# Optimization experiments

Measured on AMD Instinct MI355X. Metric: run time of the kernel, lower is better.

The kernel has to match this reference:

```python
import jax, jax.numpy as jnp
import numpy as np

N, H, C, E, R = 16384, 1024, 256, 16, 128
EPS = 1e-8


def setup_inputs() -> dict:
    key = jax.random.key(0)
    ks = jax.random.split(key, 8)
    s = 1.0 / np.sqrt(H)
    return {
        "x": jax.random.normal(ks[0], (N, H), jnp.float32),
        "Wd": jax.random.normal(ks[1], (H, C), jnp.float32) * s,
        "bd": jax.random.normal(ks[2], (C,), jnp.float32) * 0.01,
        "centroids": jax.random.uniform(ks[3], (E, C), jnp.float32),  # torch.rand
        "Wg": jax.random.normal(ks[4], (E, H, H), jnp.float32) * s,
        "bg": jax.random.normal(ks[5], (E, H), jnp.float32) * 0.01,
        "U": jax.random.normal(ks[6], (E, H, R), jnp.float32) * s,
        "V": jax.random.normal(ks[7], (E, R, H), jnp.float32) * (1.0 / np.sqrt(R)),
        "k": 2,
    }


def reference(x, Wd, bd, centroids, Wg, bg, U, V, k):
    # ---- Router ----
    distilled = jax.nn.gelu(x @ Wd + bd, approximate=False)          # [N, C]
    dn = distilled / jnp.maximum(
        jnp.linalg.norm(distilled, axis=-1, keepdims=True), EPS)
    cn = centroids / jnp.maximum(
        jnp.linalg.norm(centroids, axis=-1, keepdims=True), EPS)
    # cdist (euclidean) between dn [N,C] and cn [E,C]
    d2 = (jnp.sum(dn * dn, -1, keepdims=True)
          + jnp.sum(cn * cn, -1)[None, :]
          - 2.0 * (dn @ cn.T))                                        # [N, E]
    distances = jnp.sqrt(jnp.maximum(d2, 0.0))
    probabilities = jax.nn.softmax(-distances, axis=-1)               # [N, E]
    top_p, top_i = jax.lax.top_k(probabilities, k)                    # [N, k]
    # sparse combine weights: zero except at top-k experts
    combine = jnp.zeros((x.shape[0], E), x.dtype)
    combine = combine.at[jnp.arange(x.shape[0])[:, None], top_i].set(top_p)
    # ---- Expert dispatch: scan over experts (low-rank Highway blocks) ----
    def body(acc, params):
        Wg_e, bg_e, U_e, V_e, w_e = params
        gate = jax.nn.sigmoid(x @ Wg_e + bg_e)                        # [N, H]
        trans = (x @ U_e) @ V_e                                       # [N, H]
        y = gate * trans + (1.0 - gate) * x
        return acc + w_e[:, None] * y, None
    out, _ = jax.lax.scan(body, jnp.zeros_like(x),
                          (Wg, bg, U, V, combine.T))
    return out
```

## Files before the change

kernel.cpp:

```cpp
#include <hip/hip_runtime.h>
#include <hip/hip_bf16.h>
#include <hip/hip_fp16.h>
#include <cstdint>
#include <cstddef>

#define NTOK 16384
#define HD   1024
#define CD   256
#define NE   16
#define RD   128
#define MB2    272
#define LOGB   2176
#define EGRID  2304

typedef __attribute__((ext_vector_type(8))) short bf16x8;
typedef __attribute__((ext_vector_type(4))) float f32x4;
typedef unsigned short u16;
typedef unsigned int u32;

__device__ __forceinline__ u16 f2bf(float f) {
    u32 u = __float_as_uint(f);
    u32 r = (u + 0x7FFFu + ((u >> 16) & 1u)) >> 16;
    return (u16)r;
}

__device__ __forceinline__ void gload16(const void* g, void* lds) {
    __builtin_amdgcn_global_load_lds((const __attribute__((address_space(1))) void*)g,
                                     (__attribute__((address_space(3))) void*)lds,
                                     16, 0, 0);
}

__device__ __forceinline__ float wredsum(float v) {
#pragma unroll
    for (int m = 32; m >= 1; m >>= 1) v += __shfl_xor(v, m, 64);
    return v;
}

__global__ __launch_bounds__(64) void centroid_norm_kernel(
    const float* __restrict__ cen, float* __restrict__ cn, float* __restrict__ sncn)
{
    int e = blockIdx.x, l = threadIdx.x;
    float4 c = *(const float4*)&cen[e * CD + l * 4];
    float ss = wredsum(c.x * c.x + c.y * c.y + c.z * c.z + c.w * c.w);
    float den = fmaxf(sqrtf(ss), 1e-8f);
    float4 n;
    n.x = c.x / den; n.y = c.y / den; n.z = c.z / den; n.w = c.w / den;
    *(float4*)&cn[e * CD + l * 4] = n;
    float s2 = wredsum(n.x * n.x + n.y * n.y + n.z * n.z + n.w * n.w);
    if (l == 0) sncn[e] = s2;
}

__global__ __launch_bounds__(256, 4) void router_gemm_kernel(
    const float* __restrict__ x, const float* __restrict__ Wd,
    const float* __restrict__ bd, float* __restrict__ dT)
{
    __shared__ float lA[16][128];
    __shared__ float lB[16][64];
    int tid = threadIdx.x;
    int rb = (blockIdx.x >> 2) * 128;
    int cb = (blockIdx.x & 3) * 64;
    int tx = tid & 15, ty = tid >> 4;
    int arow = tid >> 1, akq = (tid & 1) * 8;
    int bk = tid >> 4, bc = (tid & 15) * 4;
    float acc[8][4];
#pragma unroll
    for (int i = 0; i < 8; ++i)
#pragma unroll
        for (int j = 0; j < 4; ++j) acc[i][j] = 0.f;

    for (int k0 = 0; k0 < HD; k0 += 16) {
        float4 a0 = *(const float4*)&x[(size_t)(rb + arow) * HD + k0 + akq];
        float4 a1 = *(const float4*)&x[(size_t)(rb + arow) * HD + k0 + akq + 4];
        float4 bv = *(const float4*)&Wd[(size_t)(k0 + bk) * CD + cb + bc];
        __syncthreads();
        lA[akq + 0][arow] = a0.x; lA[akq + 1][arow] = a0.y;
        lA[akq + 2][arow] = a0.z; lA[akq + 3][arow] = a0.w;
        lA[akq + 4][arow] = a1.x; lA[akq + 5][arow] = a1.y;
        lA[akq + 6][arow] = a1.z; lA[akq + 7][arow] = a1.w;
        *(float4*)&lB[bk][bc] = bv;
        __syncthreads();
#pragma unroll
        for (int kk = 0; kk < 16; ++kk) {
            float4 va0 = *(const float4*)&lA[kk][ty * 8];
            float4 va1 = *(const float4*)&lA[kk][ty * 8 + 4];
            float4 vb  = *(const float4*)&lB[kk][tx * 4];
            float ar[8] = {va0.x, va0.y, va0.z, va0.w, va1.x, va1.y, va1.z, va1.w};
            float br[4] = {vb.x, vb.y, vb.z, vb.w};
#pragma unroll
            for (int i = 0; i < 8; ++i)
#pragma unroll
                for (int j = 0; j < 4; ++j) acc[i][j] = fmaf(ar[i], br[j], acc[i][j]);
        }
    }
#pragma unroll
    for (int j = 0; j < 4; ++j) {
        int c = cb + tx * 4 + j;
        float b = bd[c];
        float g[8];
#pragma unroll
        for (int i = 0; i < 8; ++i) {
            float v = acc[i][j] + b;
            g[i] = 0.5f * v * (1.f + erff(v * 0.70710678118654752f));
        }
        float4 w0 = {g[0], g[1], g[2], g[3]};
        float4 w1 = {g[4], g[5], g[6], g[7]};
        *(float4*)&dT[(size_t)c * NTOK + rb + ty * 8] = w0;
        *(float4*)&dT[(size_t)c * NTOK + rb + ty * 8 + 4] = w1;
    }
}

__global__ __launch_bounds__(256) void router_score_kernel(
    const float* __restrict__ dT, const float* __restrict__ cn,
    const float* __restrict__ sncn, int* __restrict__ top_i,
    float* __restrict__ top_w, int* __restrict__ counts)
{
    __shared__ float lcn[NE][CD];
    __shared__ float sdot[NE][64];
    __shared__ float sss[64];
    __shared__ int hist[NE];
    int tid = threadIdx.x, lane = tid & 63, w = tid >> 6;
    for (int i = tid; i < NE * CD / 4; i += 256)
        ((float4*)&lcn[0][0])[i] = ((const float4*)cn)[i];
    if (tid < NE) hist[tid] = 0;
    __syncthreads();

    int tokbase = blockIdx.x * 64;
    const float* p = dT + tokbase + lane;
    int e0 = w * 4;
    float d0 = 0.f, d1 = 0.f, d2a = 0.f, d3 = 0.f, ss = 0.f;
#pragma unroll 4
    for (int k = 0; k < CD; ++k) {
        float v = p[(size_t)k * NTOK];
        ss = fmaf(v, v, ss);
        d0 = fmaf(v, lcn[e0 + 0][k], d0);
        d1 = fmaf(v, lcn[e0 + 1][k], d1);
        d2a = fmaf(v, lcn[e0 + 2][k], d2a);
        d3 = fmaf(v, lcn[e0 + 3][k], d3);
    }
    sdot[e0 + 0][lane] = d0;
    sdot[e0 + 1][lane] = d1;
    sdot[e0 + 2][lane] = d2a;
    sdot[e0 + 3][lane] = d3;
    if (w == 0) sss[lane] = ss;
    __syncthreads();

    if (tid < 64) {
        int tok = tokbase + tid;
        float ssv = sss[tid];
        float den = fmaxf(sqrtf(ssv), 1e-8f);
        float inv = 1.f / den;
        float sndn = (ssv * inv) * inv;
        float pr[NE];
#pragma unroll
        for (int e = 0; e < NE; ++e) {
            float dotn = sdot[e][tid] * inv;
            float dd2 = sndn + sncn[e] - 2.f * dotn;
            pr[e] = -sqrtf(fmaxf(dd2, 0.f));
        }
        float mx = pr[0];
#pragma unroll
        for (int e = 1; e < NE; ++e) mx = fmaxf(mx, pr[e]);
        float sum = 0.f;
#pragma unroll
        for (int e = 0; e < NE; ++e) { pr[e] = expf(pr[e] - mx); sum += pr[e]; }
        float invs = 1.f / sum;
#pragma unroll
        for (int e = 0; e < NE; ++e) pr[e] *= invs;
        int i1 = 0; float p1 = pr[0];
#pragma unroll
        for (int e = 1; e < NE; ++e) if (pr[e] > p1) { p1 = pr[e]; i1 = e; }
        int i2 = -1; float p2 = -1.f;
#pragma unroll
        for (int e = 0; e < NE; ++e) if (e != i1 && pr[e] > p2) { p2 = pr[e]; i2 = e; }
        top_i[tok * 2 + 0] = i1; top_w[tok * 2 + 0] = p1;
        top_i[tok * 2 + 1] = i2; top_w[tok * 2 + 1] = p2;
        atomicAdd(&hist[i1], 1);
        atomicAdd(&hist[i2], 1);
    }
    __syncthreads();
    if (tid < NE) atomicAdd(&counts[tid], hist[tid]);
}

__global__ void scan_kernel(const int* __restrict__ counts, int* __restrict__ offsets,
                            int* __restrict__ blkstart, int* __restrict__ cursor)
{
    if (threadIdx.x == 0 && blockIdx.x == 0) {
        int o = 0, b = 0;
        for (int e = 0; e < NE; ++e) {
            offsets[e] = o; blkstart[e] = b; cursor[e] = 0;
            o += counts[e]; b += (counts[e] + 127) >> 7;
        }
        offsets[NE] = o; blkstart[NE] = b;
    }
}

__global__ __launch_bounds__(256) void build_lists_kernel(
    const int* __restrict__ top_i, const float* __restrict__ top_w,
    const int* __restrict__ offsets, int* __restrict__ cursor,
    int* __restrict__ list_tok, float* __restrict__ list_w)
{
    int t = blockIdx.x * 256 + threadIdx.x;
#pragma unroll
    for (int j = 0; j < 2; ++j) {
        int e = top_i[t * 2 + j];
        int pos = atomicAdd(&cursor[e], 1);
        int idx = offsets[e] + pos;
        list_tok[idx] = t;
        list_w[idx] = top_w[t * 2 + j];
    }
}

__global__ __launch_bounds__(256) void cvt_bf16_kernel(
    const float* __restrict__ src, u16* __restrict__ dst, int n4)
{
    int i = blockIdx.x * 256 + threadIdx.x;
    if (i >= n4) return;
    float4 v = *(const float4*)&src[(size_t)i * 4];
    ushort4 o;
    o.x = f2bf(v.x); o.y = f2bf(v.y); o.z = f2bf(v.z); o.w = f2bf(v.w);
    *(ushort4*)&dst[(size_t)i * 4] = o;
}

__global__ __launch_bounds__(256) void transpose_cvt_kernel(
    const float* __restrict__ src, u16* __restrict__ dst, int K, int N)
{
    __shared__ float t[32][33];
    const float* s = src + (size_t)blockIdx.z * K * N;
    u16* d = dst + (size_t)blockIdx.z * K * N;
    int kb = blockIdx.y * 32, nb = blockIdx.x * 32;
    int r = threadIdx.x >> 3, c4 = (threadIdx.x & 7) * 4;
    float4 v = *(const float4*)&s[(size_t)(kb + r) * N + nb + c4];
    t[r][c4 + 0] = v.x; t[r][c4 + 1] = v.y; t[r][c4 + 2] = v.z; t[r][c4 + 3] = v.w;
    __syncthreads();
    ushort4 o;
    o.x = f2bf(t[c4 + 0][r]); o.y = f2bf(t[c4 + 1][r]);
    o.z = f2bf(t[c4 + 2][r]); o.w = f2bf(t[c4 + 3][r]);
    *(ushort4*)&d[(size_t)(nb + r) * K + kb + c4] = o;
}


__global__ __launch_bounds__(256, 3) void tproj_kernel(
    const u16* __restrict__ xbf, const u16* __restrict__ uT,
    const int* __restrict__ list_tok, const int* __restrict__ offsets,
    const int* __restrict__ blkstart, u16* __restrict__ tbf)
{
    __shared__ __align__(16) u16 lds[2 * 8192];
    __shared__ int s_tok[128];
    int mb = blockIdx.x;
    int e = 0;
#pragma unroll
    for (int i = 0; i < NE; ++i) if (mb >= blkstart[i + 1]) e = i + 1;
    if (e >= NE) return;
    int mloc = (mb - blkstart[e]) * 128;
    int base = offsets[e] + mloc;
    int cnt = offsets[e + 1] - offsets[e];
    int mv = min(128, cnt - mloc);
    int tid = threadIdx.x, lane = tid & 63, w = tid >> 6;
    if (tid < 128) s_tok[tid] = list_tok[base + (tid < mv ? tid : 0)];
    __syncthreads();
    int lrow = lane >> 2;
    int sl = (lane & 3) ^ ((lane >> 3) & 3);
    int rr = lane & 15, hi = lane >> 4;
    int rslot = hi ^ ((rr >> 1) & 3);
    int wr = w >> 1, wc = w & 1;
    const u16* uE = uT + (size_t)e * RD * HD;

    const u16* gb[4]; char* lp[4];
#pragma unroll
    for (int i = 0; i < 4; ++i) {
        int idx = w + 4 * i;
        if (idx < 8) {
            int row = idx * 16 + lrow;
            gb[i] = xbf + (size_t)s_tok[row] * HD + sl * 8;
            lp[i] = (char*)lds + idx * 1024;
        } else {
            int row = (idx - 8) * 16 + lrow;
            gb[i] = uE + (size_t)row * HD + sl * 8;
            lp[i] = (char*)lds + 8192 + (idx - 8) * 1024;
        }
    }
    const f32x4 zz = {0.f, 0.f, 0.f, 0.f};
    f32x4 acc[4][4];
#pragma unroll
    for (int im = 0; im < 4; ++im)
#pragma unroll
        for (int in = 0; in < 4; ++in) acc[im][in] = zz;

    auto STAGE = [&](int buf, int t) {
#pragma unroll
        for (int i = 0; i < 4; ++i) gload16(gb[i] + t * 32, lp[i] + buf * 16384);
    };
    auto COMP = [&](int buf, f32x4 (&a)[4][4]) {
        const u16* LA = lds + buf * 8192;
        const u16* LB = LA + 4096;
        bf16x8 af[4], bfv[4];
#pragma unroll
        for (int im = 0; im < 4; ++im) af[im] = *(const bf16x8*)&LA[(wr * 64 + im * 16 + rr) * 32 + rslot * 8];
#pragma unroll
        for (int in = 0; in < 4; ++in) bfv[in] = *(const bf16x8*)&LB[(wc * 64 + in * 16 + rr) * 32 + rslot * 8];
#pragma unroll
        for (int im = 0; im < 4; ++im)
#pragma unroll
            for (int in = 0; in < 4; ++in)
                a[im][in] = __builtin_amdgcn_mfma_f32_16x16x32_bf16(af[im], bfv[in], a[im][in], 0, 0, 0);
    };

    STAGE(0, 0);
    __syncthreads();
    for (int t = 0; t < 31; ++t) {
        STAGE((t + 1) & 1, t + 1);
        COMP(t & 1, acc);
        __syncthreads();
    }
    COMP(1, acc);

#pragma unroll
    for (int im = 0; im < 4; ++im)
#pragma unroll
        for (int in = 0; in < 4; ++in)
#pragma unroll
            for (int j = 0; j < 4; ++j) {
                int r = wr * 64 + im * 16 + hi * 4 + j;
                if (r < mv) {
                    int c = wc * 64 + in * 16 + rr;
                    tbf[(size_t)(base + r) * RD + c] = f2bf(acc[im][in][j]);
                }
            }
}

__global__ __launch_bounds__(256, 3) void expert_kernel(
    const u16* __restrict__ xbf, const u16* __restrict__ wgT,
    const u16* __restrict__ vT, const u16* __restrict__ tbf,
    const float* __restrict__ x, const float* __restrict__ bg,
    const int* __restrict__ list_tok, const float* __restrict__ list_w,
    const int* __restrict__ offsets, const int* __restrict__ blkstart,
    float* __restrict__ out)
{
    __shared__ __align__(16) u16 lds[2 * 8192];
    __shared__ int s_tok[128];
    __shared__ float s_w[128];
    int d = blockIdx.x;
    int l = (d >> 8) * 256 + (d & 7) * 32 + ((d & 255) >> 3);
    if (l >= LOGB) return;
    int mb = l >> 3, ct = l & 7;
    int e = 0;
#pragma unroll
    for (int i = 0; i < NE; ++i) if (mb >= blkstart[i + 1]) e = i + 1;
    if (e >= NE) return;
    int mloc = (mb - blkstart[e]) * 128;
    int base = offsets[e] + mloc;
    int cnt = offsets[e + 1] - offsets[e];
    int mv = min(128, cnt - mloc);
    int tid = threadIdx.x, lane = tid & 63, w = tid >> 6;
    if (tid < 128) {
        int p = base + (tid < mv ? tid : 0);
        s_tok[tid] = list_tok[p];
        s_w[tid] = (tid < mv) ? list_w[p] : 0.f;
    }
    __syncthreads();
    int lrow = lane >> 2;
    int sl = (lane & 3) ^ ((lane >> 3) & 3);
    int rr = lane & 15, hi = lane >> 4;
    int rslot = hi ^ ((rr >> 1) & 3);
    int wr = w >> 1, wc = w & 1;

    const u16* wgE = wgT + (size_t)e * HD * HD + (size_t)(ct * 128) * HD;
    const u16* vE  = vT  + (size_t)e * HD * RD + (size_t)(ct * 128) * RD;

    char* lp[4];
    const u16* gbT[4]; const u16* gbG[4];
#pragma unroll
    for (int i = 0; i < 4; ++i) {
        int idx = w + 4 * i;
        if (idx < 8) {
            int row = idx * 16 + lrow;
            lp[i]  = (char*)lds + idx * 1024;
            gbT[i] = tbf + (size_t)(base + (row < mv ? row : 0)) * RD + sl * 8;
            gbG[i] = xbf + (size_t)s_tok[row] * HD + sl * 8;
        } else {
            int row = (idx - 8) * 16 + lrow;
            lp[i]  = (char*)lds + 8192 + (idx - 8) * 1024;
            gbT[i] = vE  + (size_t)row * RD + sl * 8;
            gbG[i] = wgE + (size_t)row * HD + sl * 8;
        }
    }

    auto STAGE = [&](int buf, int t, const u16* const (&gb)[4]) {
#pragma unroll
        for (int i = 0; i < 4; ++i) gload16(gb[i] + t * 32, lp[i] + buf * 16384);
    };
    auto COMP = [&](int buf, f32x4 (&a)[4][4]) {
        const u16* LA = lds + buf * 8192;
        const u16* LB = LA + 4096;
        bf16x8 af[4], bfv[4];
#pragma unroll
        for (int im = 0; im < 4; ++im) af[im] = *(const bf16x8*)&LA[(wr * 64 + im * 16 + rr) * 32 + rslot * 8];
#pragma unroll
        for (int in = 0; in < 4; ++in) bfv[in] = *(const bf16x8*)&LB[(wc * 64 + in * 16 + rr) * 32 + rslot * 8];
#pragma unroll
        for (int im = 0; im < 4; ++im)
#pragma unroll
            for (int in = 0; in < 4; ++in)
                a[im][in] = __builtin_amdgcn_mfma_f32_16x16x32_bf16(af[im], bfv[in], a[im][in], 0, 0, 0);
    };

    const f32x4 zz = {0.f, 0.f, 0.f, 0.f};
    f32x4 accT[4][4];
#pragma unroll
    for (int im = 0; im < 4; ++im)
#pragma unroll
        for (int in = 0; in < 4; ++in) accT[im][in] = zz;

    STAGE(0, 0, gbT);
    __syncthreads();
#pragma unroll
    for (int s = 0; s < 4; ++s) {
        if (s < 3) STAGE((s + 1) & 1, s + 1, gbT);
        else       STAGE(0, 0, gbG);
        COMP(s & 1, accT);
        __syncthreads();
    }

    __half2 tpk[4][4][2];
#pragma unroll
    for (int im = 0; im < 4; ++im)
#pragma unroll
        for (int in = 0; in < 4; ++in) {
            tpk[im][in][0] = __floats2half2_rn(accT[im][in][0], accT[im][in][1]);
            tpk[im][in][1] = __floats2half2_rn(accT[im][in][2], accT[im][in][3]);
        }

    f32x4 accG[4][4];
#pragma unroll
    for (int im = 0; im < 4; ++im)
#pragma unroll
        for (int in = 0; in < 4; ++in) accG[im][in] = zz;

    for (int t = 0; t < 31; ++t) {
        STAGE((t + 1) & 1, t + 1, gbG);
        COMP(t & 1, accG);
        __syncthreads();
    }
    COMP(1, accG);

    float bgv[4];
#pragma unroll
    for (int in = 0; in < 4; ++in)
        bgv[in] = bg[e * HD + ct * 128 + wc * 64 + in * 16 + rr];

#pragma unroll
    for (int im = 0; im < 4; ++im)
#pragma unroll
        for (int j = 0; j < 4; ++j) {
            int r = wr * 64 + im * 16 + hi * 4 + j;
            if (r < mv) {
                int tok = s_tok[r];
                float wgt = s_w[r];
                size_t rowoff = (size_t)tok * HD;
#pragma unroll
                for (int in = 0; in < 4; ++in) {
                    int c = ct * 128 + wc * 64 + in * 16 + rr;
                    float gp = accG[im][in][j] + bgv[in];
                    float sg = 1.f / (1.f + __expf(-gp));
                    float2 tq = __half22float2(tpk[im][in][j >> 1]);
                    float tr = (j & 1) ? tq.y : tq.x;
                    float xv = x[rowoff + c];
                    float yv = sg * tr + (1.f - sg) * xv;
                    atomicAdd(&out[rowoff + c], wgt * yv);
                }
            }
        }
}

extern "C" void kernel_launch(void* const* d_in, const int* in_sizes, int n_in,
                              void* d_out, int out_size, void* d_ws, size_t ws_size,
                              hipStream_t stream)
{
    const float* x   = (const float*)d_in[0];
    const float* Wd  = (const float*)d_in[1];
    const float* bd  = (const float*)d_in[2];
    const float* cen = (const float*)d_in[3];
    const float* Wg  = (const float*)d_in[4];
    const float* bg  = (const float*)d_in[5];
    const float* U   = (const float*)d_in[6];
    const float* V   = (const float*)d_in[7];
    float* out = (float*)d_out;

    char* ws = (char*)d_ws;
    size_t off = 0;
    auto alloc = [&](size_t bytes) { size_t o = off; off = (off + bytes + 255) & ~(size_t)255; return o; };
    float* dT        = (float*)(ws + alloc((size_t)NTOK * CD * 4));
    float* cn        = (float*)(ws + alloc((size_t)NE * CD * 4));
    float* sncn      = (float*)(ws + alloc(NE * 4));
    int*   top_i     = (int*)(ws + alloc((size_t)NTOK * 2 * 4));
    float* top_w     = (float*)(ws + alloc((size_t)NTOK * 2 * 4));
    int*   counts    = (int*)(ws + alloc(NE * 4));
    int*   offsets   = (int*)(ws + alloc((NE + 1) * 4));
    int*   blkstart  = (int*)(ws + alloc((NE + 1) * 4));
    int*   cursor    = (int*)(ws + alloc(NE * 4));
    int*   list_tok  = (int*)(ws + alloc((size_t)NTOK * 2 * 4));
    float* list_w    = (float*)(ws + alloc((size_t)NTOK * 2 * 4));
    u16*   xbf       = (u16*)(ws + alloc((size_t)NTOK * HD * 2));
    u16*   wgT       = (u16*)(ws + alloc((size_t)NE * HD * HD * 2));
    u16*   uT        = (u16*)(ws + alloc((size_t)NE * RD * HD * 2));
    u16*   vT        = (u16*)(ws + alloc((size_t)NE * RD * HD * 2));
    u16*   tbf       = (u16*)(ws + alloc(((size_t)NTOK * 2 + 128) * RD * 2));

    hipMemsetAsync(out, 0, (size_t)out_size * 4, stream);
    hipMemsetAsync(counts, 0, NE * 4, stream);

    centroid_norm_kernel<<<NE, 64, 0, stream>>>(cen, cn, sncn);
    router_gemm_kernel<<<(NTOK / 128) * 4, 256, 0, stream>>>(x, Wd, bd, dT);
    router_score_kernel<<<NTOK / 64, 256, 0, stream>>>(dT, cn, sncn, top_i, top_w, counts);
    scan_kernel<<<1, 64, 0, stream>>>(counts, offsets, blkstart, cursor);
    build_lists_kernel<<<NTOK / 256, 256, 0, stream>>>(top_i, top_w, offsets, cursor, list_tok, list_w);

    cvt_bf16_kernel<<<(NTOK * HD / 4 + 255) / 256, 256, 0, stream>>>(x, xbf, NTOK * HD / 4);
    transpose_cvt_kernel<<<dim3(HD / 32, HD / 32, NE), 256, 0, stream>>>(Wg, wgT, HD, HD);
    transpose_cvt_kernel<<<dim3(RD / 32, HD / 32, NE), 256, 0, stream>>>(U, uT, HD, RD);
    transpose_cvt_kernel<<<dim3(HD / 32, RD / 32, NE), 256, 0, stream>>>(V, vT, RD, HD);

    tproj_kernel<<<MB2, 256, 0, stream>>>(xbf, uT, list_tok, offsets, blkstart, tbf);
    expert_kernel<<<EGRID, 256, 0, stream>>>(xbf, wgT, vT, tbf, x, bg,
                                             list_tok, list_w, offsets, blkstart, out);
}
```

Before: 563.4 us.

## Split expert kernel into gate GEMM and trans kernels with 256-row tiles

```diff
diff --git a/kernel.cpp b/kernel.cpp
--- a/kernel.cpp
+++ b/kernel.cpp
@@ -10,8 +10,9 @@
 #define NE   16
 #define RD   128
 #define MB2    272
-#define LOGB   2176
-#define EGRID  2304
+#define MB3    144
+#define LOGB2  1152
+#define EGRID2 1280
 
 typedef __attribute__((ext_vector_type(8))) short bf16x8;
 typedef __attribute__((ext_vector_type(4))) float f32x4;
@@ -182,15 +183,18 @@
 }
 
 __global__ void scan_kernel(const int* __restrict__ counts, int* __restrict__ offsets,
-                            int* __restrict__ blkstart, int* __restrict__ cursor)
+                            int* __restrict__ blk128, int* __restrict__ blk256,
+                            int* __restrict__ cursor)
 {
     if (threadIdx.x == 0 && blockIdx.x == 0) {
-        int o = 0, b = 0;
+        int o = 0, b1 = 0, b2 = 0;
         for (int e = 0; e < NE; ++e) {
-            offsets[e] = o; blkstart[e] = b; cursor[e] = 0;
-            o += counts[e]; b += (counts[e] + 127) >> 7;
-        }
-        offsets[NE] = o; blkstart[NE] = b;
+            offsets[e] = o; blk128[e] = b1; blk256[e] = b2; cursor[e] = 0;
+            o += counts[e];
+            b1 += (counts[e] + 127) >> 7;
+            b2 += (counts[e] + 255) >> 8;
+        }
+        offsets[NE] = o; blk128[NE] = b1; blk256[NE] = b2;
     }
 }
 
@@ -242,16 +246,16 @@
 __global__ __launch_bounds__(256, 3) void tproj_kernel(
     const u16* __restrict__ xbf, const u16* __restrict__ uT,
     const int* __restrict__ list_tok, const int* __restrict__ offsets,
-    const int* __restrict__ blkstart, u16* __restrict__ tbf)
+    const int* __restrict__ blk128, u16* __restrict__ tbf)
 {
     __shared__ __align__(16) u16 lds[2 * 8192];
     __shared__ int s_tok[128];
     int mb = blockIdx.x;
     int e = 0;
 #pragma unroll
-    for (int i = 0; i < NE; ++i) if (mb >= blkstart[i + 1]) e = i + 1;
+    for (int i = 0; i < NE; ++i) if (mb >= blk128[i + 1]) e = i + 1;
     if (e >= NE) return;
-    int mloc = (mb - blkstart[e]) * 128;
+    int mloc = (mb - blk128[e]) * 128;
     int base = offsets[e] + mloc;
     int cnt = offsets[e + 1] - offsets[e];
     int mv = min(128, cnt - mloc);
@@ -328,35 +332,28 @@
             }
 }
 
-__global__ __launch_bounds__(256, 3) void expert_kernel(
+__global__ __launch_bounds__(256, 2) void gate_kernel(
     const u16* __restrict__ xbf, const u16* __restrict__ wgT,
-    const u16* __restrict__ vT, const u16* __restrict__ tbf,
-    const float* __restrict__ x, const float* __restrict__ bg,
-    const int* __restrict__ list_tok, const float* __restrict__ list_w,
-    const int* __restrict__ offsets, const int* __restrict__ blkstart,
-    float* __restrict__ out)
-{
-    __shared__ __align__(16) u16 lds[2 * 8192];
-    __shared__ int s_tok[128];
-    __shared__ float s_w[128];
+    const float* __restrict__ bg, const int* __restrict__ list_tok,
+    const int* __restrict__ offsets, const int* __restrict__ blk256,
+    __half* __restrict__ gsig)
+{
+    __shared__ __align__(16) u16 lds[2 * 12288];
+    __shared__ int s_tok[256];
     int d = blockIdx.x;
     int l = (d >> 8) * 256 + (d & 7) * 32 + ((d & 255) >> 3);
-    if (l >= LOGB) return;
+    if (l >= LOGB2) return;
     int mb = l >> 3, ct = l & 7;
     int e = 0;
 #pragma unroll
-    for (int i = 0; i < NE; ++i) if (mb >= blkstart[i + 1]) e = i + 1;
+    for (int i = 0; i < NE; ++i) if (mb >= blk256[i + 1]) e = i + 1;
     if (e >= NE) return;
-    int mloc = (mb - blkstart[e]) * 128;
+    int mloc = (mb - blk256[e]) * 256;
     int base = offsets[e] + mloc;
     int cnt = offsets[e + 1] - offsets[e];
-    int mv = min(128, cnt - mloc);
+    int mv = min(256, cnt - mloc);
     int tid = threadIdx.x, lane = tid & 63, w = tid >> 6;
-    if (tid < 128) {
-        int p = base + (tid < mv ? tid : 0);
-        s_tok[tid] = list_tok[p];
-        s_w[tid] = (tid < mv) ? list_w[p] : 0.f;
-    }
+    s_tok[tid] = list_tok[base + (tid < mv ? tid : 0)];
     __syncthreads();
     int lrow = lane >> 2;
     int sl = (lane & 3) ^ ((lane >> 3) & 3);
@@ -365,83 +362,56 @@
     int wr = w >> 1, wc = w & 1;
 
     const u16* wgE = wgT + (size_t)e * HD * HD + (size_t)(ct * 128) * HD;
-    const u16* vE  = vT  + (size_t)e * HD * RD + (size_t)(ct * 128) * RD;
-
-    char* lp[4];
-    const u16* gbT[4]; const u16* gbG[4];
-#pragma unroll
-    for (int i = 0; i < 4; ++i) {
+
+    const u16* gb[6]; char* lp[6];
+#pragma unroll
+    for (int i = 0; i < 6; ++i) {
         int idx = w + 4 * i;
-        if (idx < 8) {
+        if (idx < 16) {
             int row = idx * 16 + lrow;
-            lp[i]  = (char*)lds + idx * 1024;
-            gbT[i] = tbf + (size_t)(base + (row < mv ? row : 0)) * RD + sl * 8;
-            gbG[i] = xbf + (size_t)s_tok[row] * HD + sl * 8;
+            gb[i] = xbf + (size_t)s_tok[row] * HD + sl * 8;
+            lp[i] = (char*)lds + idx * 1024;
         } else {
-            int row = (idx - 8) * 16 + lrow;
-            lp[i]  = (char*)lds + 8192 + (idx - 8) * 1024;
-            gbT[i] = vE  + (size_t)row * RD + sl * 8;
-            gbG[i] = wgE + (size_t)row * HD + sl * 8;
-        }
-    }
-
-    auto STAGE = [&](int buf, int t, const u16* const (&gb)[4]) {
-#pragma unroll
-        for (int i = 0; i < 4; ++i) gload16(gb[i] + t * 32, lp[i] + buf * 16384);
+            int row = (idx - 16) * 16 + lrow;
+            gb[i] = wgE + (size_t)row * HD + sl * 8;
+            lp[i] = (char*)lds + 16384 + (idx - 16) * 1024;
+        }
+    }
+
+    const f32x4 zz = {0.f, 0.f, 0.f, 0.f};
+    f32x4 acc[8][4];
+#pragma unroll
+    for (int im = 0; im < 8; ++im)
+#pragma unroll
+        for (int in = 0; in < 4; ++in) acc[im][in] = zz;
+
+    auto STAGE = [&](int buf, int t) {
+#pragma unroll
+        for (int i = 0; i < 6; ++i) gload16(gb[i] + t * 32, lp[i] + buf * 24576);
     };
-    auto COMP = [&](int buf, f32x4 (&a)[4][4]) {
-        const u16* LA = lds + buf * 8192;
-        const u16* LB = LA + 4096;
-        bf16x8 af[4], bfv[4];
-#pragma unroll
-        for (int im = 0; im < 4; ++im) af[im] = *(const bf16x8*)&LA[(wr * 64 + im * 16 + rr) * 32 + rslot * 8];
+    auto COMP = [&](int buf) {
+        const u16* LA = lds + buf * 12288;
+        const u16* LB = LA + 8192;
+        bf16x8 af[8], bfv[4];
+#pragma unroll
+        for (int im = 0; im < 8; ++im) af[im] = *(const bf16x8*)&LA[(wr * 128 + im * 16 + rr) * 32 + rslot * 8];
 #pragma unroll
         for (int in = 0; in < 4; ++in) bfv[in] = *(const bf16x8*)&LB[(wc * 64 + in * 16 + rr) * 32 + rslot * 8];
 #pragma unroll
-        for (int im = 0; im < 4; ++im)
+        for (int im = 0; im < 8; ++im)
 #pragma unroll
             for (int in = 0; in < 4; ++in)
-                a[im][in] = __builtin_amdgcn_mfma_f32_16x16x32_bf16(af[im], bfv[in], a[im][in], 0, 0, 0);
+                acc[im][in] = __builtin_amdgcn_mfma_f32_16x16x32_bf16(af[im], bfv[in], acc[im][in], 0, 0, 0);
     };
 
-    const f32x4 zz = {0.f, 0.f, 0.f, 0.f};
-    f32x4 accT[4][4];
-#pragma unroll
-    for (int im = 0; im < 4; ++im)
-#pragma unroll
-        for (int in = 0; in < 4; ++in) accT[im][in] = zz;
-
-    STAGE(0, 0, gbT);
-    __syncthreads();
-#pragma unroll
-    for (int s = 0; s < 4; ++s) {
-        if (s < 3) STAGE((s + 1) & 1, s + 1, gbT);
-        else       STAGE(0, 0, gbG);
-        COMP(s & 1, accT);
+    STAGE(0, 0);
+    __syncthreads();
+    for (int t = 0; t < 31; ++t) {
+        STAGE((t + 1) & 1, t + 1);
+        COMP(t & 1);
         __syncthreads();
     }
-
-    __half2 tpk[4][4][2];
-#pragma unroll
-    for (int im = 0; im < 4; ++im)
-#pragma unroll
-        for (int in = 0; in < 4; ++in) {
-            tpk[im][in][0] = __floats2half2_rn(accT[im][in][0], accT[im][in][1]);
-            tpk[im][in][1] = __floats2half2_rn(accT[im][in][2], accT[im][in][3]);
-        }
-
-    f32x4 accG[4][4];
-#pragma unroll
-    for (int im = 0; im < 4; ++im)
-#pragma unroll
-        for (int in = 0; in < 4; ++in) accG[im][in] = zz;
-
-    for (int t = 0; t < 31; ++t) {
-        STAGE((t + 1) & 1, t + 1, gbG);
-        COMP(t & 1, accG);
-        __syncthreads();
-    }
-    COMP(1, accG);
+    COMP(1);
 
     float bgv[4];
 #pragma unroll
@@ -449,21 +419,124 @@
         bgv[in] = bg[e * HD + ct * 128 + wc * 64 + in * 16 + rr];
 
 #pragma unroll
-    for (int im = 0; im < 4; ++im)
+    for (int im = 0; im < 8; ++im)
 #pragma unroll
         for (int j = 0; j < 4; ++j) {
-            int r = wr * 64 + im * 16 + hi * 4 + j;
+            int r = wr * 128 + im * 16 + hi * 4 + j;
+            if (r < mv) {
+#pragma unroll
+                for (int in = 0; in < 4; ++in) {
+                    int c = ct * 128 + wc * 64 + in * 16 + rr;
+                    float sg = 1.f / (1.f + __expf(-(acc[im][in][j] + bgv[in])));
+                    gsig[(size_t)(base + r) * HD + c] = __float2half(sg);
+                }
+            }
+        }
+}
+
+__global__ __launch_bounds__(256, 2) void trans_kernel(
+    const u16* __restrict__ tbf, const u16* __restrict__ vT,
+    const __half* __restrict__ gsig, const float* __restrict__ x,
+    const int* __restrict__ list_tok, const float* __restrict__ list_w,
+    const int* __restrict__ offsets, const int* __restrict__ blk256,
+    float* __restrict__ out)
+{
+    __shared__ __align__(16) u16 lds[2 * 12288];
+    __shared__ int s_tok[256];
+    __shared__ float s_w[256];
+    int d = blockIdx.x;
+    int l = (d >> 8) * 256 + (d & 7) * 32 + ((d & 255) >> 3);
+    if (l >= LOGB2) return;
+    int mb = l >> 3, ct = l & 7;
+    int e = 0;
+#pragma unroll
+    for (int i = 0; i < NE; ++i) if (mb >= blk256[i + 1]) e = i + 1;
+    if (e >= NE) return;
+    int mloc = (mb - blk256[e]) * 256;
+    int base = offsets[e] + mloc;
+    int cnt = offsets[e + 1] - offsets[e];
+    int mv = min(256, cnt - mloc);
+    int tid = threadIdx.x, lane = tid & 63, w = tid >> 6;
+    {
+        int p = base + (tid < mv ? tid : 0);
+        s_tok[tid] = list_tok[p];
+        s_w[tid] = (tid < mv) ? list_w[p] : 0.f;
+    }
+    __syncthreads();
+    int lrow = lane >> 2;
+    int sl = (lane & 3) ^ ((lane >> 3) & 3);
+    int rr = lane & 15, hi = lane >> 4;
+    int rslot = hi ^ ((rr >> 1) & 3);
+    int wr = w >> 1, wc = w & 1;
+
+    const u16* vE = vT + (size_t)e * HD * RD + (size_t)(ct * 128) * RD;
+
+    const u16* gb[6]; char* lp[6];
+#pragma unroll
+    for (int i = 0; i < 6; ++i) {
+        int idx = w + 4 * i;
+        if (idx < 16) {
+            int row = idx * 16 + lrow;
+            gb[i] = tbf + (size_t)(base + (row < mv ? row : 0)) * RD + sl * 8;
+            lp[i] = (char*)lds + idx * 1024;
+        } else {
+            int row = (idx - 16) * 16 + lrow;
+            gb[i] = vE + (size_t)row * RD + sl * 8;
+            lp[i] = (char*)lds + 16384 + (idx - 16) * 1024;
+        }
+    }
+
+    const f32x4 zz = {0.f, 0.f, 0.f, 0.f};
+    f32x4 acc[8][4];
+#pragma unroll
+    for (int im = 0; im < 8; ++im)
+#pragma unroll
+        for (int in = 0; in < 4; ++in) acc[im][in] = zz;
+
+    auto STAGE = [&](int buf, int t) {
+#pragma unroll
+        for (int i = 0; i < 6; ++i) gload16(gb[i] + t * 32, lp[i] + buf * 24576);
+    };
+    auto COMP = [&](int buf) {
+        const u16* LA = lds + buf * 12288;
+        const u16* LB = LA + 8192;
+        bf16x8 af[8], bfv[4];
+#pragma unroll
+        for (int im = 0; im < 8; ++im) af[im] = *(const bf16x8*)&LA[(wr * 128 + im * 16 + rr) * 32 + rslot * 8];
+#pragma unroll
+        for (int in = 0; in < 4; ++in) bfv[in] = *(const bf16x8*)&LB[(wc * 64 + in * 16 + rr) * 32 + rslot * 8];
+#pragma unroll
+        for (int im = 0; im < 8; ++im)
+#pragma unroll
+            for (int in = 0; in < 4; ++in)
+                acc[im][in] = __builtin_amdgcn_mfma_f32_16x16x32_bf16(af[im], bfv[in], acc[im][in], 0, 0, 0);
+    };
+
+    STAGE(0, 0);
+    __syncthreads();
+#pragma unroll
+    for (int t = 0; t < 3; ++t) {
+        STAGE((t + 1) & 1, t + 1);
+        COMP(t & 1);
+        __syncthreads();
+    }
+    COMP(1);
+
+#pragma unroll
+    for (int im = 0; im < 8; ++im)
+#pragma unroll
+        for (int j = 0; j < 4; ++j) {
+            int r = wr * 128 + im * 16 + hi * 4 + j;
             if (r < mv) {
                 int tok = s_tok[r];
                 float wgt = s_w[r];
                 size_t rowoff = (size_t)tok * HD;
+                size_t grow = (size_t)(base + r) * HD;
 #pragma unroll
                 for (int in = 0; in < 4; ++in) {
                     int c = ct * 128 + wc * 64 + in * 16 + rr;
-                    float gp = accG[im][in][j] + bgv[in];
-                    float sg = 1.f / (1.f + __expf(-gp));
-                    float2 tq = __half22float2(tpk[im][in][j >> 1]);
-                    float tr = (j & 1) ? tq.y : tq.x;
+                    float sg = __half2float(gsig[grow + c]);
+                    float tr = acc[im][in][j];
                     float xv = x[rowoff + c];
                     float yv = sg * tr + (1.f - sg) * xv;
                     atomicAdd(&out[rowoff + c], wgt * yv);
@@ -496,7 +569,8 @@
     float* top_w     = (float*)(ws + alloc((size_t)NTOK * 2 * 4));
     int*   counts    = (int*)(ws + alloc(NE * 4));
     int*   offsets   = (int*)(ws + alloc((NE + 1) * 4));
-    int*   blkstart  = (int*)(ws + alloc((NE + 1) * 4));
+    int*   blk128    = (int*)(ws + alloc((NE + 1) * 4));
+    int*   blk256    = (int*)(ws + alloc((NE + 1) * 4));
     int*   cursor    = (int*)(ws + alloc(NE * 4));
     int*   list_tok  = (int*)(ws + alloc((size_t)NTOK * 2 * 4));
     float* list_w    = (float*)(ws + alloc((size_t)NTOK * 2 * 4));
@@ -504,7 +578,8 @@
     u16*   wgT       = (u16*)(ws + alloc((size_t)NE * HD * HD * 2));
     u16*   uT        = (u16*)(ws + alloc((size_t)NE * RD * HD * 2));
     u16*   vT        = (u16*)(ws + alloc((size_t)NE * RD * HD * 2));
-    u16*   tbf       = (u16*)(ws + alloc(((size_t)NTOK * 2 + 128) * RD * 2));
+    u16*   tbf       = (u16*)(ws + alloc(((size_t)NTOK * 2 + 256) * RD * 2));
+    __half* gsig     = (__half*)(ws + alloc(((size_t)NTOK * 2 + 256) * HD * 2));
 
     hipMemsetAsync(out, 0, (size_t)out_size * 4, stream);
     hipMemsetAsync(counts, 0, NE * 4, stream);
@@ -512,7 +587,7 @@
     centroid_norm_kernel<<<NE, 64, 0, stream>>>(cen, cn, sncn);
     router_gemm_kernel<<<(NTOK / 128) * 4, 256, 0, stream>>>(x, Wd, bd, dT);
     router_score_kernel<<<NTOK / 64, 256, 0, stream>>>(dT, cn, sncn, top_i, top_w, counts);
-    scan_kernel<<<1, 64, 0, stream>>>(counts, offsets, blkstart, cursor);
+    scan_kernel<<<1, 64, 0, stream>>>(counts, offsets, blk128, blk256, cursor);
     build_lists_kernel<<<NTOK / 256, 256, 0, stream>>>(top_i, top_w, offsets, cursor, list_tok, list_w);
 
     cvt_bf16_kernel<<<(NTOK * HD / 4 + 255) / 256, 256, 0, stream>>>(x, xbf, NTOK * HD / 4);
@@ -520,7 +595,8 @@
     transpose_cvt_kernel<<<dim3(RD / 32, HD / 32, NE), 256, 0, stream>>>(U, uT, HD, RD);
     transpose_cvt_kernel<<<dim3(HD / 32, RD / 32, NE), 256, 0, stream>>>(V, vT, RD, HD);
 
-    tproj_kernel<<<MB2, 256, 0, stream>>>(xbf, uT, list_tok, offsets, blkstart, tbf);
-    expert_kernel<<<EGRID, 256, 0, stream>>>(xbf, wgT, vT, tbf, x, bg,
-                                             list_tok, list_w, offsets, blkstart, out);
-}
+    tproj_kernel<<<MB2, 256, 0, stream>>>(xbf, uT, list_tok, offsets, blk128, tbf);
+    gate_kernel<<<EGRID2, 256, 0, stream>>>(xbf, wgT, bg, list_tok, offsets, blk256, gsig);
+    trans_kernel<<<EGRID2, 256, 0, stream>>>(tbf, vT, gsig, x, list_tok, list_w,
+                                             offsets, blk256, out);
+}
```

After: 691.2 us. 1.23x slower.

## Run router GEMM on bf16 MFMA with hi/lo split emulating fp32 precision

Applied to the files above, without the earlier changes.

```diff
diff --git a/kernel.cpp b/kernel.cpp
--- a/kernel.cpp
+++ b/kernel.cpp
@@ -22,6 +22,10 @@
     u32 u = __float_as_uint(f);
     u32 r = (u + 0x7FFFu + ((u >> 16) & 1u)) >> 16;
     return (u16)r;
+}
+__device__ __forceinline__ float bf2f(u16 h) {
+    u32 u = ((u32)h) << 16;
+    return __uint_as_float(u);
 }
 
 __device__ __forceinline__ void gload16(const void* g, void* lds) {
@@ -50,63 +54,156 @@
     if (l == 0) sncn[e] = s2;
 }
 
-__global__ __launch_bounds__(256, 4) void router_gemm_kernel(
-    const float* __restrict__ x, const float* __restrict__ Wd,
+__global__ __launch_bounds__(256) void cvt_split_kernel(
+    const float* __restrict__ src, u16* __restrict__ hi, u16* __restrict__ lo, int n4)
+{
+    int i = blockIdx.x * 256 + threadIdx.x;
+    if (i >= n4) return;
+    float4 v = *(const float4*)&src[(size_t)i * 4];
+    ushort4 h, l;
+    h.x = f2bf(v.x); h.y = f2bf(v.y); h.z = f2bf(v.z); h.w = f2bf(v.w);
+    l.x = f2bf(v.x - bf2f(h.x)); l.y = f2bf(v.y - bf2f(h.y));
+    l.z = f2bf(v.z - bf2f(h.z)); l.w = f2bf(v.w - bf2f(h.w));
+    *(ushort4*)&hi[(size_t)i * 4] = h;
+    *(ushort4*)&lo[(size_t)i * 4] = l;
+}
+
+__global__ __launch_bounds__(256) void transpose_cvt_kernel(
+    const float* __restrict__ src, u16* __restrict__ dst, int K, int N)
+{
+    __shared__ float t[32][33];
+    const float* s = src + (size_t)blockIdx.z * K * N;
+    u16* d = dst + (size_t)blockIdx.z * K * N;
+    int kb = blockIdx.y * 32, nb = blockIdx.x * 32;
+    int r = threadIdx.x >> 3, c4 = (threadIdx.x & 7) * 4;
+    float4 v = *(const float4*)&s[(size_t)(kb + r) * N + nb + c4];
+    t[r][c4 + 0] = v.x; t[r][c4 + 1] = v.y; t[r][c4 + 2] = v.z; t[r][c4 + 3] = v.w;
+    __syncthreads();
+    ushort4 o;
+    o.x = f2bf(t[c4 + 0][r]); o.y = f2bf(t[c4 + 1][r]);
+    o.z = f2bf(t[c4 + 2][r]); o.w = f2bf(t[c4 + 3][r]);
+    *(ushort4*)&d[(size_t)(nb + r) * K + kb + c4] = o;
+}
+
+__global__ __launch_bounds__(256) void transpose_cvt_split_kernel(
+    const float* __restrict__ src, u16* __restrict__ dh, u16* __restrict__ dl,
+    int K, int N)
+{
+    __shared__ float t[32][33];
+    int kb = blockIdx.y * 32, nb = blockIdx.x * 32;
+    int r = threadIdx.x >> 3, c4 = (threadIdx.x & 7) * 4;
+    float4 v = *(const float4*)&src[(size_t)(kb + r) * N + nb + c4];
+    t[r][c4 + 0] = v.x; t[r][c4 + 1] = v.y; t[r][c4 + 2] = v.z; t[r][c4 + 3] = v.w;
+    __syncthreads();
+    float f0 = t[c4 + 0][r], f1 = t[c4 + 1][r], f2 = t[c4 + 2][r], f3 = t[c4 + 3][r];
+    ushort4 h, l;
+    h.x = f2bf(f0); h.y = f2bf(f1); h.z = f2bf(f2); h.w = f2bf(f3);
+    l.x = f2bf(f0 - bf2f(h.x)); l.y = f2bf(f1 - bf2f(h.y));
+    l.z = f2bf(f2 - bf2f(h.z)); l.w = f2bf(f3 - bf2f(h.w));
+    *(ushort4*)&dh[(size_t)(nb + r) * K + kb + c4] = h;
+    *(ushort4*)&dl[(size_t)(nb + r) * K + kb + c4] = l;
+}
+
+
+__global__ __launch_bounds__(256, 2) void router_mfma_kernel(
+    const u16* __restrict__ xh, const u16* __restrict__ xl,
+    const u16* __restrict__ wdh, const u16* __restrict__ wdl,
     const float* __restrict__ bd, float* __restrict__ dT)
 {
-    __shared__ float lA[16][128];
-    __shared__ float lB[16][64];
-    int tid = threadIdx.x;
-    int rb = (blockIdx.x >> 2) * 128;
-    int cb = (blockIdx.x & 3) * 64;
-    int tx = tid & 15, ty = tid >> 4;
-    int arow = tid >> 1, akq = (tid & 1) * 8;
-    int bk = tid >> 4, bc = (tid & 15) * 4;
-    float acc[8][4];
-#pragma unroll
-    for (int i = 0; i < 8; ++i)
-#pragma unroll
-        for (int j = 0; j < 4; ++j) acc[i][j] = 0.f;
-
-    for (int k0 = 0; k0 < HD; k0 += 16) {
-        float4 a0 = *(const float4*)&x[(size_t)(rb + arow) * HD + k0 + akq];
-        float4 a1 = *(const float4*)&x[(size_t)(rb + arow) * HD + k0 + akq + 4];
-        float4 bv = *(const float4*)&Wd[(size_t)(k0 + bk) * CD + cb + bc];
+    __shared__ __align__(16) u16 lds[2 * 16384];
+    int rb = (blockIdx.x >> 1) * 128;
+    int cb = (blockIdx.x & 1) * 128;
+    int tid = threadIdx.x, lane = tid & 63, w = tid >> 6;
+    int lrow = lane >> 2;
+    int sl = (lane & 3) ^ ((lane >> 3) & 3);
+    int rr = lane & 15, hi = lane >> 4;
+    int rslot = hi ^ ((rr >> 1) & 3);
+    int wr = w >> 1, wc = w & 1;
+
+    const u16* gb[8]; char* lp[8];
+#pragma unroll
+    for (int i = 0; i < 8; ++i) {
+        int idx = w + 4 * i;
+        int sub = idx & 7;
+        int row = sub * 16 + lrow;
+        if (idx < 8) {
+            gb[i] = xh + (size_t)(rb + row) * HD + sl * 8;
+            lp[i] = (char*)lds + idx * 1024;
+        } else if (idx < 16) {
+            gb[i] = xl + (size_t)(rb + row) * HD + sl * 8;
+            lp[i] = (char*)lds + 8192 + sub * 1024;
+        } else if (idx < 24) {
+            gb[i] = wdh + (size_t)(cb + row) * HD + sl * 8;
+            lp[i] = (char*)lds + 16384 + sub * 1024;
+        } else {
+            gb[i] = wdl + (size_t)(cb + row) * HD + sl * 8;
+            lp[i] = (char*)lds + 24576 + sub * 1024;
+        }
+    }
+
+    const f32x4 zz = {0.f, 0.f, 0.f, 0.f};
+    f32x4 acc[4][4];
+#pragma unroll
+    for (int im = 0; im < 4; ++im)
+#pragma unroll
+        for (int in = 0; in < 4; ++in) acc[im][in] = zz;
+
+    auto STAGE = [&](int buf, int t) {
+#pragma unroll
+        for (int i = 0; i < 8; ++i) gload16(gb[i] + t * 32, lp[i] + buf * 32768);
+    };
+    auto COMP = [&](int buf) {
+        const u16* LXH = lds + buf * 16384;
+        const u16* LXL = LXH + 4096;
+        const u16* LWH = LXH + 8192;
+        const u16* LWL = LXH + 12288;
+        bf16x8 ah[4], al[4], bh[4], bl[4];
+#pragma unroll
+        for (int im = 0; im < 4; ++im) {
+            int row = wr * 64 + im * 16 + rr;
+            ah[im] = *(const bf16x8*)&LXH[row * 32 + rslot * 8];
+            al[im] = *(const bf16x8*)&LXL[row * 32 + rslot * 8];
+        }
+#pragma unroll
+        for (int in = 0; in < 4; ++in) {
+            int row = wc * 64 + in * 16 + rr;
+            bh[in] = *(const bf16x8*)&LWH[row * 32 + rslot * 8];
+            bl[in] = *(const bf16x8*)&LWL[row * 32 + rslot * 8];
+        }
+#pragma unroll
+        for (int im = 0; im < 4; ++im)
+#pragma unroll
+            for (int in = 0; in < 4; ++in) {
+                acc[im][in] = __builtin_amdgcn_mfma_f32_16x16x32_bf16(ah[im], bh[in], acc[im][in], 0, 0, 0);
+                acc[im][in] = __builtin_amdgcn_mfma_f32_16x16x32_bf16(ah[im], bl[in], acc[im][in], 0, 0, 0);
+                acc[im][in] = __builtin_amdgcn_mfma_f32_16x16x32_bf16(al[im], bh[in], acc[im][in], 0, 0, 0);
+            }
+    };
+
+    STAGE(0, 0);
+    __syncthreads();
+    for (int t = 0; t < 31; ++t) {
+        STAGE((t + 1) & 1, t + 1);
+        COMP(t & 1);
         __syncthreads();
-        lA[akq + 0][arow] = a0.x; lA[akq + 1][arow] = a0.y;
-        lA[akq + 2][arow] = a0.z; lA[akq + 3][arow] = a0.w;
-        lA[akq + 4][arow] = a1.x; lA[akq + 5][arow] = a1.y;
-        lA[akq + 6][arow] = a1.z; lA[akq + 7][arow] = a1.w;
-        *(float4*)&lB[bk][bc] = bv;
-        __syncthreads();
-#pragma unroll
-        for (int kk = 0; kk < 16; ++kk) {
-            float4 va0 = *(const float4*)&lA[kk][ty * 8];
-            float4 va1 = *(const float4*)&lA[kk][ty * 8 + 4];
-            float4 vb  = *(const float4*)&lB[kk][tx * 4];
-            float ar[8] = {va0.x, va0.y, va0.z, va0.w, va1.x, va1.y, va1.z, va1.w};
-            float br[4] = {vb.x, vb.y, vb.z, vb.w};
-#pragma unroll
-            for (int i = 0; i < 8; ++i)
-#pragma unroll
-                for (int j = 0; j < 4; ++j) acc[i][j] = fmaf(ar[i], br[j], acc[i][j]);
-        }
-    }
-#pragma unroll
-    for (int j = 0; j < 4; ++j) {
-        int c = cb + tx * 4 + j;
-        float b = bd[c];
-        float g[8];
-#pragma unroll
-        for (int i = 0; i < 8; ++i) {
-            float v = acc[i][j] + b;
-            g[i] = 0.5f * v * (1.f + erff(v * 0.70710678118654752f));
-        }
-        float4 w0 = {g[0], g[1], g[2], g[3]};
-        float4 w1 = {g[4], g[5], g[6], g[7]};
-        *(float4*)&dT[(size_t)c * NTOK + rb + ty * 8] = w0;
-        *(float4*)&dT[(size_t)c * NTOK + rb + ty * 8 + 4] = w1;
-    }
+    }
+    COMP(1);
+
+#pragma unroll
+    for (int im = 0; im < 4; ++im)
+#pragma unroll
+        for (int in = 0; in < 4; ++in) {
+            int c = cb + wc * 64 + in * 16 + rr;
+            float b = bd[c];
+            float g[4];
+#pragma unroll
+            for (int j = 0; j < 4; ++j) {
+                float v = acc[im][in][j] + b;
+                g[j] = 0.5f * v * (1.f + erff(v * 0.70710678118654752f));
+            }
+            float4 o = {g[0], g[1], g[2], g[3]};
+            *(float4*)&dT[(size_t)c * NTOK + rb + wr * 64 + im * 16 + hi * 4] = o;
+        }
 }
 
 __global__ __launch_bounds__(256) void router_score_kernel(
@@ -209,35 +306,6 @@
         list_w[idx] = top_w[t * 2 + j];
     }
 }
-
-__global__ __launch_bounds__(256) void cvt_bf16_kernel(
-    const float* __restrict__ src, u16* __restrict__ dst, int n4)
-{
-    int i = blockIdx.x * 256 + threadIdx.x;
-    if (i >= n4) return;
-    float4 v = *(const float4*)&src[(size_t)i * 4];
-    ushort4 o;
-    o.x = f2bf(v.x); o.y = f2bf(v.y); o.z = f2bf(v.z); o.w = f2bf(v.w);
-    *(ushort4*)&dst[(size_t)i * 4] = o;
-}
-
-__global__ __launch_bounds__(256) void transpose_cvt_kernel(
-    const float* __restrict__ src, u16* __restrict__ dst, int K, int N)
-{
-    __shared__ float t[32][33];
-    const float* s = src + (size_t)blockIdx.z * K * N;
-    u16* d = dst + (size_t)blockIdx.z * K * N;
-    int kb = blockIdx.y * 32, nb = blockIdx.x * 32;
-    int r = threadIdx.x >> 3, c4 = (threadIdx.x & 7) * 4;
-    float4 v = *(const float4*)&s[(size_t)(kb + r) * N + nb + c4];
-    t[r][c4 + 0] = v.x; t[r][c4 + 1] = v.y; t[r][c4 + 2] = v.z; t[r][c4 + 3] = v.w;
-    __syncthreads();
-    ushort4 o;
-    o.x = f2bf(t[c4 + 0][r]); o.y = f2bf(t[c4 + 1][r]);
-    o.z = f2bf(t[c4 + 2][r]); o.w = f2bf(t[c4 + 3][r]);
-    *(ushort4*)&d[(size_t)(nb + r) * K + kb + c4] = o;
-}
-
 
 __global__ __launch_bounds__(256, 3) void tproj_kernel(
     const u16* __restrict__ xbf, const u16* __restrict__ uT,
@@ -501,6 +569,9 @@
     int*   list_tok  = (int*)(ws + alloc((size_t)NTOK * 2 * 4));
     float* list_w    = (float*)(ws + alloc((size_t)NTOK * 2 * 4));
     u16*   xbf       = (u16*)(ws + alloc((size_t)NTOK * HD * 2));
+    u16*   xlo       = (u16*)(ws + alloc((size_t)NTOK * HD * 2));
+    u16*   wdh       = (u16*)(ws + alloc((size_t)CD * HD * 2));
+    u16*   wdl       = (u16*)(ws + alloc((size_t)CD * HD * 2));
     u16*   wgT       = (u16*)(ws + alloc((size_t)NE * HD * HD * 2));
     u16*   uT        = (u16*)(ws + alloc((size_t)NE * RD * HD * 2));
     u16*   vT        = (u16*)(ws + alloc((size_t)NE * RD * HD * 2));
@@ -510,12 +581,13 @@
     hipMemsetAsync(counts, 0, NE * 4, stream);
 
     centroid_norm_kernel<<<NE, 64, 0, stream>>>(cen, cn, sncn);
-    router_gemm_kernel<<<(NTOK / 128) * 4, 256, 0, stream>>>(x, Wd, bd, dT);
+    cvt_split_kernel<<<(NTOK * HD / 4 + 255) / 256, 256, 0, stream>>>(x, xbf, xlo, NTOK * HD / 4);
+    transpose_cvt_split_kernel<<<dim3(CD / 32, HD / 32), 256, 0, stream>>>(Wd, wdh, wdl, HD, CD);
+    router_mfma_kernel<<<(NTOK / 128) * 2, 256, 0, stream>>>(xbf, xlo, wdh, wdl, bd, dT);
     router_score_kernel<<<NTOK / 64, 256, 0, stream>>>(dT, cn, sncn, top_i, top_w, counts);
     scan_kernel<<<1, 64, 0, stream>>>(counts, offsets, blkstart, cursor);
     build_lists_kernel<<<NTOK / 256, 256, 0, stream>>>(top_i, top_w, offsets, cursor, list_tok, list_w);
 
-    cvt_bf16_kernel<<<(NTOK * HD / 4 + 255) / 256, 256, 0, stream>>>(x, xbf, NTOK * HD / 4);
     transpose_cvt_kernel<<<dim3(HD / 32, HD / 32, NE), 256, 0, stream>>>(Wg, wgT, HD, HD);
     transpose_cvt_kernel<<<dim3(RD / 32, HD / 32, NE), 256, 0, stream>>>(U, uT, HD, RD);
     transpose_cvt_kernel<<<dim3(HD / 32, RD / 32, NE), 256, 0, stream>>>(V, vT, RD, HD);
```

Measured after the change: 503.6 us. 10.6% less time.
